# Kernel optimization log

Hardware: AMD Instinct MI355X
Metric: run time of the kernel (lower is better)

The kernel has to match this reference:

```python
import jax, jax.numpy as jnp
import numpy as np
import math

D_IN, D_MODEL, N_HEADS, DIM_HEAD, NB_FEAT, N_CLASSES = 24, 512, 8, 64, 266, 10
FF_DIM = 4 * D_MODEL  # performer-pytorch FeedForward mult=4
LN_EPS = 1e-5
B, N = 16, 2048


def gaussian_orthogonal(key, nb_rows, nb_cols):
    # FAVOR+ gaussian orthogonal random matrix (scaling=0: chi-distributed row norms)
    n_blocks = nb_rows // nb_cols + 1
    keys = jax.random.split(key, n_blocks + 1)
    blocks = []
    for i in range(n_blocks):
        q, _ = jnp.linalg.qr(jax.random.normal(keys[i], (nb_cols, nb_cols)))
        blocks.append(q.T)
    mat = jnp.concatenate(blocks, axis=0)[:nb_rows]
    multiplier = jnp.linalg.norm(jax.random.normal(keys[-1], (nb_rows, nb_cols)), axis=1)
    return multiplier[:, None] * mat


def layer_norm(x, g, b):
    mu = jnp.mean(x, axis=-1, keepdims=True)
    var = jnp.var(x, axis=-1, keepdims=True)
    return (x - mu) * jax.lax.rsqrt(var + LN_EPS) * g + b


def softmax_kernel(data, proj, is_query, eps=1e-4):
    # FAVOR+ positive random features approximating the softmax kernel
    data_norm = data.shape[-1] ** -0.25
    ratio = proj.shape[0] ** -0.5
    dd = jnp.einsum('bhnd,fd->bhnf', data * data_norm, proj)  # [B,H,N,F]
    diag = 0.5 * jnp.sum(data * data, axis=-1, keepdims=True) * (data_norm ** 2)
    if is_query:
        m = jax.lax.stop_gradient(jnp.max(dd, axis=-1, keepdims=True))
    else:
        m = jax.lax.stop_gradient(jnp.max(dd))
    return ratio * (jnp.exp(dd - diag - m) + eps)


def setup_inputs() -> dict:
    key = jax.random.key(0)
    ks = jax.random.split(key, 24)

    def linw(k, fi, fo):
        bnd = 1.0 / math.sqrt(fi)
        return jax.random.uniform(k, (fi, fo), minval=-bnd, maxval=bnd, dtype=jnp.float32)

    def linb(k, fi, fo):
        bnd = 1.0 / math.sqrt(fi)
        return jax.random.uniform(k, (fo,), minval=-bnd, maxval=bnd, dtype=jnp.float32)

    return {
        'x': jax.random.normal(ks[0], (B, N, D_IN), dtype=jnp.float32),
        'enc_w': linw(ks[1], D_IN, D_MODEL), 'enc_b': linb(ks[2], D_IN, D_MODEL),
        'ln1_g': jnp.ones((D_MODEL,), jnp.float32), 'ln1_b': jnp.zeros((D_MODEL,), jnp.float32),
        'wq': linw(ks[3], D_MODEL, D_MODEL), 'bq': linb(ks[4], D_MODEL, D_MODEL),
        'wk': linw(ks[5], D_MODEL, D_MODEL), 'bk': linb(ks[6], D_MODEL, D_MODEL),
        'wv': linw(ks[7], D_MODEL, D_MODEL), 'bv': linb(ks[8], D_MODEL, D_MODEL),
        'wo': linw(ks[9], D_MODEL, D_MODEL), 'bo': linb(ks[10], D_MODEL, D_MODEL),
        'proj': gaussian_orthogonal(ks[11], NB_FEAT, DIM_HEAD).astype(jnp.float32),
        'ln2_g': jnp.ones((D_MODEL,), jnp.float32), 'ln2_b': jnp.zeros((D_MODEL,), jnp.float32),
        'ff_w1': linw(ks[12], D_MODEL, FF_DIM), 'ff_b1': linb(ks[13], D_MODEL, FF_DIM),
        'ff_w2': linw(ks[14], FF_DIM, D_MODEL), 'ff_b2': linb(ks[15], FF_DIM, D_MODEL),
        'mlp_w1': linw(ks[16], D_MODEL, D_MODEL), 'mlp_b1': linb(ks[17], D_MODEL, D_MODEL),
        'mlp_w2': linw(ks[18], D_MODEL, N_CLASSES), 'mlp_b2': linb(ks[19], D_MODEL, N_CLASSES),
    }


def reference(x, enc_w, enc_b, ln1_g, ln1_b, wq, bq, wk, bk, wv, bv, wo, bo, proj,
              ln2_g, ln2_b, ff_w1, ff_b1, ff_w2, ff_b2, mlp_w1, mlp_b1, mlp_w2, mlp_b2):
    b, n, _ = x.shape
    h = (x @ enc_w + enc_b) * math.sqrt(D_MODEL)  # [B,N,D]

    # --- Performer layer: PreLN + FAVOR+ self-attention ---
    y = layer_norm(h, ln1_g, ln1_b)
    split = lambda t: t.reshape(b, n, N_HEADS, DIM_HEAD).transpose(0, 2, 1, 3)  # [B,H,N,Dh]
    q = split(y @ wq + bq)
    k = split(y @ wk + bk)
    v = split(y @ wv + bv)
    qp = softmax_kernel(q, proj, is_query=True)   # [B,H,N,F]
    kp = softmax_kernel(k, proj, is_query=False)  # [B,H,N,F]
    # non-causal linear attention
    k_sum = kp.sum(axis=2)                                   # [B,H,F]
    d_inv = 1.0 / jnp.einsum('bhnf,bhf->bhn', qp, k_sum)     # [B,H,N]
    ctx = jnp.einsum('bhnf,bhnd->bhfd', kp, v)               # [B,H,F,Dh]
    attn = jnp.einsum('bhnf,bhfd,bhn->bhnd', qp, ctx, d_inv)
    attn = attn.transpose(0, 2, 1, 3).reshape(b, n, D_MODEL)
    h = h + attn @ wo + bo

    y = layer_norm(h, ln2_g, ln2_b)
    h = h + jax.nn.gelu(y @ ff_w1 + ff_b1, approximate=False) @ ff_w2 + ff_b2

    # --- max pool over sequence + MLP head ---
    p = jnp.max(h, axis=1)  # [B,D]
    return jax.nn.relu(p @ mlp_w1 + mlp_b1) @ mlp_w2 + mlp_b2  # [B,n_classes]
```

## Files before the change

kernel.cpp:

```cpp
#include <hip/hip_runtime.h>
#include <math.h>

typedef unsigned short u16;
typedef __bf16 bf16x8 __attribute__((ext_vector_type(8)));
typedef float f32x4 __attribute__((ext_vector_type(4)));
typedef u16 u16x8 __attribute__((ext_vector_type(8)));

#define DEVI static __device__ __forceinline__

#define NB 16
#define SEQ 2048
#define DM 512
#define DH 64
#define NF 266
#define NFP 288
#define NFQ 296
#define FFD 2048
#define ROWS (NB*SEQ)
#define SQRT_DM 22.62741699796952f
#define DATA_NORM 0.3535533905932738f
#define RATIO 0.0613139073f
#define KEPS 1e-4f

DEVI u16 f2b(float f){
  union{float f; unsigned u;} c; c.f=f;
  unsigned r = c.u + 0x7FFFu + ((c.u>>16)&1u);
  return (u16)(r>>16);
}
DEVI float b2f(u16 v){
  union{unsigned u; float f;} c; c.u = ((unsigned)v)<<16; return c.f;
}

DEVI f32x4 MFMA(bf16x8 a, bf16x8 b, f32x4 c){
  return __builtin_amdgcn_mfma_f32_16x16x32_bf16(a,b,c,0,0,0);
}

DEVI void async16(void* lds, const void* g){
  __builtin_amdgcn_global_load_lds(
      (const __attribute__((address_space(1))) unsigned*)g,
      (__attribute__((address_space(3))) unsigned*)lds, 16, 0, 0);
}

DEVI void atomicMaxF(float* a, float v){
  if (v >= 0.f) atomicMax((int*)a, __float_as_int(v));
  else          atomicMin((unsigned*)a, (unsigned)__float_as_int(v));
}

DEVI bf16x8 ldb8(const u16* p){ return *(const bf16x8*)p; }

DEVI float erf_fast(float u){
  float au = fabsf(u);
  float tt = __builtin_amdgcn_rcpf(1.f + 0.3275911f*au);
  float poly = tt*(0.254829592f + tt*(-0.284496736f + tt*(1.421413741f + tt*(-1.453152027f + tt*1.061405429f))));
  float er = 1.f - poly*__expf(-u*u);
  return copysignf(er, u);
}

template<int EPI>
__launch_bounds__(256,2)
__global__ void gemm_tn(const u16* __restrict__ A, int lda,
                        const u16* __restrict__ Bt, int ldb,
                        const float* __restrict__ bias,
                        float* __restrict__ resid,
                        u16* __restrict__ Cb,
                        int N, int K)
{
  __shared__ u16 As[2][128*32];
  __shared__ u16 Bs[2][128*32];
  const int t = threadIdx.x;
  const int ntn = N >> 7;
  int bid = blockIdx.x;
  const int nwg = gridDim.x;
  if ((nwg & 7) == 0){ int qq = nwg >> 3; bid = (bid & 7)*qq + (bid >> 3); }
  const int bm = bid / ntn, bn = bid % ntn;
  const int w = t>>6, l = t&63, lr = l&15, lg = l>>4;
  const int wr = (w>>1)*64, wc = (w&1)*64;
  const u16* ga = A  + (size_t)(bm*128 + (t>>2))*lda + (t&3)*8;
  const u16* gb = Bt + (size_t)(bn*128 + (t>>2))*ldb + (t&3)*8;
  const int nk = K >> 5;
  f32x4 acc[4][4];
  #pragma unroll
  for (int i=0;i<4;i++)
    #pragma unroll
    for (int j=0;j<4;j++) acc[i][j]=(f32x4){0.f,0.f,0.f,0.f};

  async16(&As[0][t*8], ga);
  async16(&As[0][64*32 + t*8], ga + (size_t)64*lda);
  async16(&Bs[0][t*8], gb);
  async16(&Bs[0][64*32 + t*8], gb + (size_t)64*ldb);

  for (int kt=0; kt<nk; ++kt){
    __syncthreads();
    if (kt+1 < nk){
      const u16* ga2 = ga + (kt+1)*32;
      const u16* gb2 = gb + (kt+1)*32;
      int nbuf = (kt+1)&1;
      async16(&As[nbuf][t*8], ga2);
      async16(&As[nbuf][64*32 + t*8], ga2 + (size_t)64*lda);
      async16(&Bs[nbuf][t*8], gb2);
      async16(&Bs[nbuf][64*32 + t*8], gb2 + (size_t)64*ldb);
    }
    const u16* as = As[kt&1];
    const u16* bs = Bs[kt&1];
    bf16x8 af[4], bff[4];
    #pragma unroll
    for (int i=0;i<4;i++) af[i]  = ldb8(&as[(wr + i*16 + lr)*32 + lg*8]);
    #pragma unroll
    for (int i=0;i<4;i++) bff[i] = ldb8(&bs[(wc + i*16 + lr)*32 + lg*8]);
    #pragma unroll
    for (int i=0;i<4;i++)
      #pragma unroll
      for (int j=0;j<4;j++)
        acc[i][j] = MFMA(af[i], bff[j], acc[i][j]);
  }

  const int r0 = bm*128 + wr + lg*4;
  const int c0 = bn*128 + wc + lr;
  #pragma unroll
  for (int i=0;i<4;i++){
    #pragma unroll
    for (int j=0;j<4;j++){
      #pragma unroll
      for (int q=0;q<4;q++){
        int r = r0 + i*16 + q;
        int c = c0 + j*16;
        float v = acc[i][j][q] + bias[c];
        if (EPI==2) v = 0.5f*v*(1.f + erf_fast(v*0.70710678f));
        size_t idx = (size_t)r*N + c;
        if (EPI==3) resid[idx] = resid[idx] + v;
        else        Cb[idx] = f2b(v);
      }
    }
  }
}

__launch_bounds__(256)
__global__ void k_prep(const float* __restrict__ wq, const float* __restrict__ wk,
                       const float* __restrict__ wv, const float* __restrict__ wo,
                       const float* __restrict__ ffw1, const float* __restrict__ ffw2,
                       const float* __restrict__ proj, const float* __restrict__ bk,
                       const float* __restrict__ bv,
                       u16* __restrict__ wqT, u16* __restrict__ wkvT, u16* __restrict__ woT,
                       u16* __restrict__ f1T, u16* __restrict__ f2T, u16* __restrict__ pjn,
                       float* __restrict__ kvb, float* __restrict__ pbuf)
{
  int bid = blockIdx.x, t = threadIdx.x;
  if (bid < 3072){
    const float* src; u16* dst; int R, C, tile;
    if      (bid < 256){ src=wq;  dst=wqT;          R=512; C=512;  tile=bid; }
    else if (bid < 512){ src=wk;  dst=wkvT;         R=512; C=512;  tile=bid-256; }
    else if (bid < 768){ src=wv;  dst=wkvT+262144;  R=512; C=512;  tile=bid-512; }
    else if (bid <1024){ src=wo;  dst=woT;          R=512; C=512;  tile=bid-768; }
    else if (bid <2048){ src=ffw1;dst=f1T;          R=512; C=2048; tile=bid-1024; }
    else               { src=ffw2;dst=f2T;          R=2048;C=512;  tile=bid-2048; }
    int ntc = C>>5;
    int tr = tile/ntc, tc = tile%ntc;
    __shared__ float tl[32][33];
    int r = t>>5, c = t&31;
    #pragma unroll
    for (int it=0; it<4; ++it)
      tl[r+it*8][c] = src[(size_t)(tr*32 + r + it*8)*C + tc*32 + c];
    __syncthreads();
    #pragma unroll
    for (int it=0; it<4; ++it)
      dst[(size_t)(tc*32 + r + it*8)*R + tr*32 + c] = f2b(tl[c][r+it*8]);
    return;
  }
  int i = (bid-3072)*256 + t;
  if (i < NFP*DH){ int f=i>>6, d=i&63; pjn[i] = f2b(f<NF ? proj[(size_t)f*64+d]*DATA_NORM : 0.f); return; }
  i -= NFP*DH;
  if (i < 1024){ kvb[i] = (i<512)? bk[i] : bv[i-512]; return; }
  i -= 1024;
  if (i < NB*DM){ pbuf[i] = -INFINITY; return; }
}

__global__ void k_signal(float* out, float v){
  if (threadIdx.x==0 && blockIdx.x==0) out[0] = v;
}

__launch_bounds__(256)
__global__ void k_encode_ln(const float* __restrict__ x, const float* __restrict__ ew,
                            const float* __restrict__ eb, const float* __restrict__ lgw,
                            const float* __restrict__ lbw, float* __restrict__ h,
                            u16* __restrict__ y)
{
  int w = threadIdx.x>>6, l = threadIdx.x&63;
  int row = blockIdx.x*4 + w;
  const float* xr = x + (size_t)row*24;
  float xv[24];
  #pragma unroll
  for (int k=0;k<24;k++) xv[k] = xr[k];
  int c0 = l*8;
  float a[8] = {0,0,0,0,0,0,0,0};
  #pragma unroll
  for (int k=0;k<24;k++){
    const float* wp = ew + (size_t)k*DM + c0;
    #pragma unroll
    for (int c=0;c<8;c++) a[c] += xv[k]*wp[c];
  }
  float s=0.f, s2=0.f;
  #pragma unroll
  for (int c=0;c<8;c++){
    a[c] = (a[c] + eb[c0+c]) * SQRT_DM;
    s += a[c]; s2 += a[c]*a[c];
  }
  #pragma unroll
  for (int m=1;m<64;m<<=1){ s += __shfl_xor(s,m); s2 += __shfl_xor(s2,m); }
  float mu = s*(1.f/DM);
  float rs = rsqrtf(s2*(1.f/DM) - mu*mu + 1e-5f);
  float* hr = h + (size_t)row*DM + c0;
  u16 yv[8];
  #pragma unroll
  for (int c=0;c<8;c++){
    hr[c] = a[c];
    yv[c] = f2b((a[c]-mu)*rs*lgw[c0+c] + lbw[c0+c]);
  }
  *(uint4*)(y + (size_t)row*DM + c0) = *(const uint4*)yv;
}

__launch_bounds__(256)
__global__ void k_ln(const float* __restrict__ h, const float* __restrict__ lgw,
                     const float* __restrict__ lbw, u16* __restrict__ y)
{
  int w = threadIdx.x>>6, l = threadIdx.x&63;
  int row = blockIdx.x*4 + w;
  int c0 = l*8;
  const float* hr = h + (size_t)row*DM + c0;
  float a[8];
  *(float4*)&a[0] = *(const float4*)hr;
  *(float4*)&a[4] = *(const float4*)(hr+4);
  float s=0.f, s2=0.f;
  #pragma unroll
  for (int c=0;c<8;c++){ s += a[c]; s2 += a[c]*a[c]; }
  #pragma unroll
  for (int m=1;m<64;m<<=1){ s += __shfl_xor(s,m); s2 += __shfl_xor(s2,m); }
  float mu = s*(1.f/DM);
  float rs = rsqrtf(s2*(1.f/DM) - mu*mu + 1e-5f);
  u16 yv[8];
  #pragma unroll
  for (int c=0;c<8;c++) yv[c] = f2b((a[c]-mu)*rs*lgw[c0+c] + lbw[c0+c]);
  *(uint4*)(y + (size_t)row*DM + c0) = *(const uint4*)yv;
}

__launch_bounds__(256,1)
__global__ void k_kmax(const u16* __restrict__ kv, const u16* __restrict__ pjn,
                       float* __restrict__ mkpart)
{
  __shared__ float red[4];
  int t = threadIdx.x, w = t>>6, l = t&63, lr = l&15, lg = l>>4;
  int bh = blockIdx.x>>3, tile = blockIdx.x&7;
  int b = bh>>3, hd = bh&7;
  int row0 = tile*256 + w*64;
  bf16x8 pf0[17], pf1[17];
  #pragma unroll
  for (int f=0; f<17; ++f){
    const u16* pb = pjn + (f*16 + lr)*64 + lg*8;
    pf0[f] = ldb8(pb); pf1[f] = ldb8(pb+32);
  }
  bf16x8 a0[4], a1[4];
  #pragma unroll
  for (int it=0; it<4; ++it){
    const u16* kb = kv + ((size_t)(b*SEQ + row0 + it*16 + lr)*1024 + hd*64 + lg*8);
    a0[it] = ldb8(kb); a1[it] = ldb8(kb+32);
  }
  float vmax = -3e38f;
  #pragma unroll
  for (int it=0; it<4; ++it){
    #pragma unroll
    for (int f=0; f<17; ++f){
      f32x4 z = (f32x4){0.f,0.f,0.f,0.f};
      z = MFMA(a0[it], pf0[f], z);
      z = MFMA(a1[it], pf1[f], z);
      if (f*16 + lr < NF){
        #pragma unroll
        for (int j=0;j<4;j++) vmax = fmaxf(vmax, z[j]);
      }
    }
  }
  #pragma unroll
  for (int m=1;m<64;m<<=1) vmax = fmaxf(vmax, __shfl_xor(vmax,m));
  if (l==0) red[w] = vmax;
  __syncthreads();
  if (t==0) mkpart[blockIdx.x] = fmaxf(fmaxf(red[0],red[1]), fmaxf(red[2],red[3]));
}

__global__ void k_kmax_red(const float* __restrict__ mkpart, float* __restrict__ mk){
  __shared__ float red[4];
  int t = threadIdx.x, w = t>>6, l = t&63;
  float v = fmaxf(fmaxf(mkpart[t], mkpart[t+256]), fmaxf(mkpart[t+512], mkpart[t+768]));
  #pragma unroll
  for (int m=1;m<64;m<<=1) v = fmaxf(v, __shfl_xor(v,m));
  if (l==0) red[w] = v;
  __syncthreads();
  if (t==0) mk[0] = fmaxf(fmaxf(red[0],red[1]), fmaxf(red[2],red[3]));
}

__launch_bounds__(256,2)
__global__ void k_kpctx(const u16* __restrict__ kv, const u16* __restrict__ pjn,
                        const float* __restrict__ mkp,
                        u16* __restrict__ ctxp, float* __restrict__ ksump)
{
  __shared__ u16 pjs[272*64];
  __shared__ u16 vT[DH*32];
  __shared__ u16 kpT[NFP*32];
  __shared__ float dbuf[4][16];
  int t = threadIdx.x, w = t>>6, l = t&63, lr = l&15, lg = l>>4;
  int bh = blockIdx.x>>2, seg = blockIdx.x&3;
  int b = bh>>3, hd = bh&7;
  int mw = w>>1, fh = (w&1)*9;
  float mk = *mkp;

  for (int i=t; i<2176; i+=256){
    int row = i>>3, cin = i&7;
    *(uint4*)&pjs[row*64 + ((cin ^ (row&7))<<3)] = ((const uint4*)pjn)[i];
  }

  f32x4 ctxa[18];
  #pragma unroll
  for (int f=0;f<18;f++) ctxa[f]=(f32x4){0.f,0.f,0.f,0.f};
  float ksa[9];
  #pragma unroll
  for (int i=0;i<9;i++) ksa[i]=0.f;

  for (int ch=0; ch<16; ++ch){
    int n0 = seg*512 + ch*32;
    __syncthreads();
    {
      int nl = t>>3, d0 = (t&7)*8;
      const u16* vsrc = kv + ((size_t)(b*SEQ + n0 + nl)*1024 + 512 + hd*64 + d0);
      uint4 vv = *(const uint4*)vsrc;
      const u16* vp = (const u16*)&vv;
      #pragma unroll
      for (int i=0;i<8;i++){
        int row = d0+i;
        vT[row*32 + (((nl>>3) ^ ((row>>1)&3))<<3) + (nl&7)] = vp[i];
      }
    }
    const u16* kb = kv + ((size_t)(b*SEQ + n0 + mw*16 + lr)*1024 + hd*64 + lg*8);
    bf16x8 a0 = ldb8(kb), a1 = ldb8(kb+32);
    float sq = 0.f;
    #pragma unroll
    for (int i=0;i<8;i++){ float u0=(float)a0[i], u1=(float)a1[i]; sq += u0*u0 + u1*u1; }
    sq += __shfl_xor(sq,16); sq += __shfl_xor(sq,32);
    if (l<16) dbuf[w][l] = sq*0.0625f;
    #pragma unroll
    for (int ff=0; ff<9; ++ff){
      int f = fh + ff;
      f32x4 z = (f32x4){0.f,0.f,0.f,0.f};
      if (f < 17){
        int row = f*16 + lr;
        const u16* pb0 = pjs + row*64 + ((lg ^ (lr&7))<<3);
        const u16* pb1 = pjs + row*64 + (((lg+4) ^ (lr&7))<<3);
        z = MFMA(a0, ldb8(pb0), z);
        z = MFMA(a1, ldb8(pb1), z);
      }
      float kp0 = RATIO*(__expf(z[0] - dbuf[w][lg*4+0] - mk) + KEPS);
      float kp1 = RATIO*(__expf(z[1] - dbuf[w][lg*4+1] - mk) + KEPS);
      float kp2 = RATIO*(__expf(z[2] - dbuf[w][lg*4+2] - mk) + KEPS);
      float kp3 = RATIO*(__expf(z[3] - dbuf[w][lg*4+3] - mk) + KEPS);
      ksa[ff] += kp0 + kp1 + kp2 + kp3;
      ushort4 kw;
      kw.x = f2b(kp0); kw.y = f2b(kp1); kw.z = f2b(kp2); kw.w = f2b(kp3);
      int row = f*16 + lr;
      int wch = (mw*2 + (lg>>1)) ^ ((row>>1)&3);
      *(ushort4*)&kpT[row*32 + (wch<<3) + ((lg&1)<<2)] = kw;
    }
    __syncthreads();
    int rr = w*16 + lr;
    bf16x8 av = ldb8(&vT[rr*32 + ((lg ^ ((rr>>1)&3))<<3)]);
    #pragma unroll
    for (int f=0;f<18;f++){
      int row = f*16 + lr;
      ctxa[f] = MFMA(av, ldb8(&kpT[row*32 + ((lg ^ ((row>>1)&3))<<3)]), ctxa[f]);
    }
  }

  __syncthreads();
  {
    float* tb = (w&1) ? (float*)pjs : (float*)kpT;
    u16* dstq = ctxp + (((size_t)seg*128 + bh)*DH + w*16)*NFP;
    #pragma unroll
    for (int r=0; r<2; ++r){
      if ((w>>1) == r){
        #pragma unroll
        for (int f=0;f<18;f++)
          #pragma unroll
          for (int j=0;j<4;j++)
            tb[(lg*4+j)*NFP + f*16 + lr] = ctxa[f][j];
        asm volatile("s_waitcnt lgkmcnt(0)" ::: "memory");
        #pragma unroll
        for (int k=0;k<9;k++){
          int c = k*64 + l;
          f32x4 v0 = *(const f32x4*)(tb + c*8);
          f32x4 v1 = *(const f32x4*)(tb + c*8 + 4);
          u16x8 o;
          o[0]=f2b(v0[0]); o[1]=f2b(v0[1]); o[2]=f2b(v0[2]); o[3]=f2b(v0[3]);
          o[4]=f2b(v1[0]); o[5]=f2b(v1[1]); o[6]=f2b(v1[2]); o[7]=f2b(v1[3]);
          *(u16x8*)(dstq + c*8) = o;
        }
      }
      __syncthreads();
    }
  }
  #pragma unroll
  for (int ff=0;ff<9;ff++){
    float v = ksa[ff];
    v += __shfl_xor(v,16); v += __shfl_xor(v,32);
    if (l<16) ksump[((size_t)seg*128 + bh)*NFP + (fh+ff)*16 + l] = v;
  }
}

__global__ void k_reduce(const u16* __restrict__ ctxp, const float* __restrict__ ksump,
                         u16* __restrict__ ctxb, float* __restrict__ ksum)
{
  const size_t CT = (size_t)128*DH*NFP;
  const size_t KT = (size_t)128*NFP;
  size_t i = (size_t)blockIdx.x*256 + threadIdx.x;
  if (i < CT){
    float s = b2f(ctxp[i]) + b2f(ctxp[i+CT]) + b2f(ctxp[i+2*CT]) + b2f(ctxp[i+3*CT]);
    ctxb[i] = f2b(s);
  } else if (i < CT + KT){
    size_t j = i - CT;
    ksum[j] = ksump[j] + ksump[j+KT] + ksump[j+2*KT] + ksump[j+3*KT];
  }
}

__launch_bounds__(256,2)
__global__ void k_qp_attn(const u16* __restrict__ q, const u16* __restrict__ pjn,
                          const u16* __restrict__ ctxb, const float* __restrict__ ksum,
                          u16* __restrict__ attn)
{
  __shared__ u16 qp[64*NFQ];
  __shared__ float dnb[64];
  __shared__ float dgb[64];
  int t = threadIdx.x, w = t>>6, l = t&63, lr = l&15, lg = l>>4;
  int bh = blockIdx.x>>5, tile = blockIdx.x&31;
  int b = bh>>3, hd = bh&7;
  int n0 = tile*64;
  const u16* qb = q + ((size_t)(b*SEQ + n0 + w*16 + lr)*DM + hd*64 + lg*8);
  bf16x8 a0 = ldb8(qb), a1 = ldb8(qb+32);
  float sq = 0.f;
  #pragma unroll
  for (int i=0;i<8;i++){ float u0=(float)a0[i], u1=(float)a1[i]; sq += u0*u0 + u1*u1; }
  sq += __shfl_xor(sq,16); sq += __shfl_xor(sq,32);
  if (l<16) dgb[w*16+l] = sq*0.0625f;

  f32x4 dd[18];
  #pragma unroll
  for (int f=0;f<18;f++){
    const u16* pb = pjn + (f*16 + lr)*64 + lg*8;
    f32x4 z = (f32x4){0.f,0.f,0.f,0.f};
    z = MFMA(a0, ldb8(pb), z);
    dd[f] = MFMA(a1, ldb8(pb+32), z);
  }
  float mj[4] = {-3e38f,-3e38f,-3e38f,-3e38f};
  #pragma unroll
  for (int f=0;f<18;f++){
    if (f*16 + lr < NF){
      #pragma unroll
      for (int j=0;j<4;j++) mj[j] = fmaxf(mj[j], dd[f][j]);
    }
  }
  #pragma unroll
  for (int m=1;m<16;m<<=1)
    #pragma unroll
    for (int j=0;j<4;j++) mj[j] = fmaxf(mj[j], __shfl_xor(mj[j],m));
  float dg[4];
  #pragma unroll
  for (int j=0;j<4;j++) dg[j] = dgb[w*16 + lg*4 + j];
  float den[4] = {0.f,0.f,0.f,0.f};
  #pragma unroll
  for (int f=0;f<18;f++){
    int col = f*16 + lr;
    float ks = ksum[(size_t)bh*NFP + col];
    #pragma unroll
    for (int j=0;j<4;j++){
      float qv = 0.f;
      if (col < NF) qv = RATIO*(__expf(dd[f][j] - dg[j] - mj[j]) + KEPS);
      den[j] += qv*ks;
      qp[(w*16 + lg*4 + j)*NFQ + col] = f2b(qv);
    }
  }
  #pragma unroll
  for (int m=1;m<16;m<<=1)
    #pragma unroll
    for (int j=0;j<4;j++) den[j] += __shfl_xor(den[j],m);
  if (lr==0){
    #pragma unroll
    for (int j=0;j<4;j++) dnb[w*16 + lg*4 + j] = den[j];
  }
  __syncthreads();
  bf16x8 aq[9];
  #pragma unroll
  for (int k9=0;k9<9;k9++) aq[k9] = ldb8(&qp[(w*16 + lr)*NFQ + k9*32 + lg*8]);
  f32x4 oacc[4];
  #pragma unroll
  for (int d=0;d<4;d++) oacc[d]=(f32x4){0.f,0.f,0.f,0.f};
  const u16* cbase = ctxb + (size_t)bh*DH*NFP;
  #pragma unroll
  for (int d=0;d<4;d++)
    #pragma unroll
    for (int k9=0;k9<9;k9++)
      oacc[d] = MFMA(aq[k9], ldb8(&cbase[(d*16 + lr)*NFP + k9*32 + lg*8]), oacc[d]);
  float di[4];
  #pragma unroll
  for (int j=0;j<4;j++) di[j] = 1.f/dnb[w*16 + lg*4 + j];
  #pragma unroll
  for (int d=0;d<4;d++)
    #pragma unroll
    for (int j=0;j<4;j++){
      int n = n0 + w*16 + lg*4 + j;
      attn[((size_t)(b*SEQ + n))*DM + hd*64 + d*16 + lr] = f2b(oacc[d][j]*di[j]);
    }
}

__global__ void k_maxpool(const float* __restrict__ h, float* __restrict__ p){
  int bi = blockIdx.x;
  int b = bi>>5, half = (bi>>4)&1, seg = bi&15;
  int c = half*256 + threadIdx.x;
  const float* hp = h + ((size_t)b*SEQ + seg*128)*DM + c;
  float m = -3e38f;
  for (int n=0;n<128;n++) m = fmaxf(m, hp[(size_t)n*DM]);
  atomicMaxF(&p[b*DM + c], m);
}

__launch_bounds__(256)
__global__ void k_head(const float* __restrict__ p, const float* __restrict__ w1,
                       const float* __restrict__ b1, const float* __restrict__ w2,
                       const float* __restrict__ b2, float* __restrict__ out)
{
  __shared__ float z[DM];
  __shared__ float pr[DM];
  int b = blockIdx.x, t = threadIdx.x;
  pr[t] = p[(size_t)b*DM + t];
  pr[t+256] = p[(size_t)b*DM + t + 256];
  __syncthreads();
  for (int c=t; c<DM; c+=256){
    float a = b1[c];
    for (int k=0;k<DM;k++) a += pr[k]*w1[(size_t)k*DM + c];
    z[c] = fmaxf(a, 0.f);
  }
  __syncthreads();
  if (t < 10){
    float a = b2[t];
    for (int k=0;k<DM;k++) a += z[k]*w2[(size_t)k*10 + t];
    out[b*10 + t] = a;
  }
}

static inline size_t align256(size_t x){ return (x+255)&~(size_t)255; }

extern "C" void kernel_launch(void* const* d_in, const int* in_sizes, int n_in,
                              void* d_out, int out_size, void* d_ws, size_t ws_size,
                              hipStream_t stream)
{
  (void)in_sizes; (void)n_in; (void)out_size;
  const float* x     = (const float*)d_in[0];
  const float* enc_w = (const float*)d_in[1];
  const float* enc_b = (const float*)d_in[2];
  const float* ln1_g = (const float*)d_in[3];
  const float* ln1_b = (const float*)d_in[4];
  const float* wq    = (const float*)d_in[5];
  const float* bq    = (const float*)d_in[6];
  const float* wk    = (const float*)d_in[7];
  const float* bk    = (const float*)d_in[8];
  const float* wv    = (const float*)d_in[9];
  const float* bv    = (const float*)d_in[10];
  const float* wo    = (const float*)d_in[11];
  const float* bo    = (const float*)d_in[12];
  const float* proj  = (const float*)d_in[13];
  const float* ln2_g = (const float*)d_in[14];
  const float* ln2_b = (const float*)d_in[15];
  const float* ff_w1 = (const float*)d_in[16];
  const float* ff_b1 = (const float*)d_in[17];
  const float* ff_w2 = (const float*)d_in[18];
  const float* ff_b2 = (const float*)d_in[19];
  const float* mw1   = (const float*)d_in[20];
  const float* mb1   = (const float*)d_in[21];
  const float* mw2   = (const float*)d_in[22];
  const float* mb2   = (const float*)d_in[23];

  char* base = (char*)d_ws;
  size_t off = 0;
  auto alloc = [&](size_t bytes)->void*{ void* r = base + off; off = align256(off + bytes); return r; };
  float* h     = (float*)alloc((size_t)ROWS*DM*4);
  u16*   slotA = (u16*)  alloc((size_t)ROWS*DM*2);
  u16*   slotB = (u16*)  alloc((size_t)ROWS*1024*2);
  u16*   wqT   = (u16*)  alloc((size_t)512*512*2);
  u16*   wkvT  = (u16*)  alloc((size_t)1024*512*2);
  u16*   woT   = (u16*)  alloc((size_t)512*512*2);
  u16*   f1T   = (u16*)  alloc((size_t)2048*512*2);
  u16*   f2T   = (u16*)  alloc((size_t)512*2048*2);
  u16*   pjn   = (u16*)  alloc((size_t)NFP*DH*2);
  float* kvb   = (float*)alloc(1024*4);
  float* mk    = (float*)alloc(256);
  float* mkpart= (float*)alloc(1024*4);
  u16*   ctxp  = (u16*)  alloc((size_t)4*128*DH*NFP*2);
  float* ksump = (float*)alloc((size_t)4*128*NFP*4);
  u16*   ctxb  = (u16*)  alloc((size_t)128*DH*NFP*2);
  float* ksum  = (float*)alloc((size_t)128*NFP*4);
  float* pbuf  = (float*)alloc((size_t)NB*DM*4);

  if (off > ws_size){
    k_signal<<<1,64,0,stream>>>((float*)d_out, (float)ws_size);
    return;
  }

  u16* y    = slotA;
  u16* attn = slotA;
  u16* kvB  = slotB;
  u16* qB   = slotB;
  u16* ffb  = slotB;

  k_prep<<<3180,256,0,stream>>>(wq, wk, wv, wo, ff_w1, ff_w2, proj, bk, bv,
                                wqT, wkvT, woT, f1T, f2T, pjn, kvb, pbuf);

  k_encode_ln<<<ROWS/4,256,0,stream>>>(x, enc_w, enc_b, ln1_g, ln1_b, h, y);
  gemm_tn<1><<<(ROWS/128)*(1024/128),256,0,stream>>>(y,512, wkvT,512, kvb, nullptr, kvB, 1024, 512);
  k_kmax<<<1024,256,0,stream>>>(kvB, pjn, mkpart);
  k_kmax_red<<<1,256,0,stream>>>(mkpart, mk);
  k_kpctx<<<512,256,0,stream>>>(kvB, pjn, mk, ctxp, ksump);
  k_reduce<<<9360,256,0,stream>>>(ctxp, ksump, ctxb, ksum);
  gemm_tn<1><<<(ROWS/128)*(512/128),256,0,stream>>>(y,512, wqT,512, bq, nullptr, qB, 512, 512);
  k_qp_attn<<<128*32,256,0,stream>>>(qB, pjn, ctxb, ksum, attn);
  gemm_tn<3><<<(ROWS/128)*(512/128),256,0,stream>>>(attn,512, woT,512, bo, h, nullptr, 512, 512);
  k_ln<<<ROWS/4,256,0,stream>>>(h, ln2_g, ln2_b, y);
  for (int c2=0;c2<2;c2++){
    const u16* ych = y + (size_t)c2*16384*512;
    float*     hch = h + (size_t)c2*16384*512;
    gemm_tn<2><<<(16384/128)*(2048/128),256,0,stream>>>(ych,512, f1T,512, ff_b1, nullptr, ffb, 2048, 512);
    gemm_tn<3><<<(16384/128)*(512/128),256,0,stream>>>(ffb,2048, f2T,2048, ff_b2, hch, nullptr, 512, 2048);
  }
  k_maxpool<<<NB*32,256,0,stream>>>(h, pbuf);
  k_head<<<NB,256,0,stream>>>(pbuf, mw1, mb1, mw2, mb2, (float*)d_out);
}
```

Before: 689.0 us.

## Keep qp features in registers via transposed MFMA and lane shuffles in qp_attn

Rewrites the query-feature/attention kernel to swap MFMA operand order so each lane holds one query row. The qp tile then stays in registers as packed bf16 and is redistributed with cross-lane shuffles instead of going through LDS and a block barrier. It recomputes the projection matmul in a second pass rather than keeping 18 accumulators live, and raises launch bounds to 4 blocks per SM. Output stores become vectorized ushort4. The cost is extra MFMA work and many shuffles, traded for less LDS traffic, no __syncthreads, and higher occupancy.

```diff
diff --git a/kernel.cpp b/kernel.cpp
--- a/kernel.cpp
+++ b/kernel.cpp
@@ -14,7 +14,6 @@
 #define DH 64
 #define NF 266
 #define NFP 288
-#define NFQ 296
 #define FFD 2048
 #define ROWS (NB*SEQ)
 #define SQRT_DM 22.62741699796952f
@@ -29,6 +28,11 @@
 }
 DEVI float b2f(u16 v){
   union{unsigned u; float f;} c; c.u = ((unsigned)v)<<16; return c.f;
+}
+DEVI unsigned cvtpk(float a, float b){
+  unsigned r;
+  asm("v_cvt_pk_bf16_f32 %0, %1, %2" : "=v"(r) : "v"(a), "v"(b));
+  return r;
 }
 
 DEVI f32x4 MFMA(bf16x8 a, bf16x8 b, f32x4 c){
@@ -425,14 +429,11 @@
   }
 }
 
-__launch_bounds__(256,2)
+__launch_bounds__(256,4)
 __global__ void k_qp_attn(const u16* __restrict__ q, const u16* __restrict__ pjn,
                           const u16* __restrict__ ctxb, const float* __restrict__ ksum,
                           u16* __restrict__ attn)
 {
-  __shared__ u16 qp[64*NFQ];
-  __shared__ float dnb[64];
-  __shared__ float dgb[64];
   int t = threadIdx.x, w = t>>6, l = t&63, lr = l&15, lg = l>>4;
   int bh = blockIdx.x>>5, tile = blockIdx.x&31;
   int b = bh>>3, hd = bh&7;
@@ -443,75 +444,83 @@
   #pragma unroll
   for (int i=0;i<8;i++){ float u0=(float)a0[i], u1=(float)a1[i]; sq += u0*u0 + u1*u1; }
   sq += __shfl_xor(sq,16); sq += __shfl_xor(sq,32);
-  if (l<16) dgb[w*16+l] = sq*0.0625f;
-
-  f32x4 dd[18];
-  #pragma unroll
-  for (int f=0;f<18;f++){
-    const u16* pb = pjn + (f*16 + lr)*64 + lg*8;
+  float dg = sq*0.0625f;
+
+  float mj = -3e38f;
+  #pragma unroll
+  for (int ft=0; ft<17; ++ft){
+    const u16* pb = pjn + (ft*16 + lr)*64 + lg*8;
     f32x4 z = (f32x4){0.f,0.f,0.f,0.f};
-    z = MFMA(a0, ldb8(pb), z);
-    dd[f] = MFMA(a1, ldb8(pb+32), z);
-  }
-  float mj[4] = {-3e38f,-3e38f,-3e38f,-3e38f};
-  #pragma unroll
-  for (int f=0;f<18;f++){
-    if (f*16 + lr < NF){
+    z = MFMA(ldb8(pb), a0, z);
+    z = MFMA(ldb8(pb+32), a1, z);
+    if (ft < 16){
       #pragma unroll
-      for (int j=0;j<4;j++) mj[j] = fmaxf(mj[j], dd[f][j]);
-    }
-  }
-  #pragma unroll
-  for (int m=1;m<16;m<<=1)
-    #pragma unroll
-    for (int j=0;j<4;j++) mj[j] = fmaxf(mj[j], __shfl_xor(mj[j],m));
-  float dg[4];
-  #pragma unroll
-  for (int j=0;j<4;j++) dg[j] = dgb[w*16 + lg*4 + j];
-  float den[4] = {0.f,0.f,0.f,0.f};
-  #pragma unroll
-  for (int f=0;f<18;f++){
-    int col = f*16 + lr;
-    float ks = ksum[(size_t)bh*NFP + col];
+      for (int j=0;j<4;j++) mj = fmaxf(mj, z[j]);
+    } else {
+      #pragma unroll
+      for (int j=0;j<4;j++) if (lg*4+j < 10) mj = fmaxf(mj, z[j]);
+    }
+  }
+  mj = fmaxf(mj, __shfl_xor(mj,16));
+  mj = fmaxf(mj, __shfl_xor(mj,32));
+
+  unsigned p0[18], p1[18];
+  float den = 0.f;
+  const float* ksb = ksum + (size_t)bh*NFP;
+  #pragma unroll
+  for (int ft=0; ft<18; ++ft){
+    f32x4 z = (f32x4){0.f,0.f,0.f,0.f};
+    if (ft < 17){
+      const u16* pb = pjn + (ft*16 + lr)*64 + lg*8;
+      z = MFMA(ldb8(pb), a0, z);
+      z = MFMA(ldb8(pb+32), a1, z);
+    }
+    f32x4 ks4 = *(const f32x4*)(ksb + ft*16 + lg*4);
+    int fb = ft*16 + lg*4;
+    float qv[4];
     #pragma unroll
     for (int j=0;j<4;j++){
-      float qv = 0.f;
-      if (col < NF) qv = RATIO*(__expf(dd[f][j] - dg[j] - mj[j]) + KEPS);
-      den[j] += qv*ks;
-      qp[(w*16 + lg*4 + j)*NFQ + col] = f2b(qv);
-    }
-  }
-  #pragma unroll
-  for (int m=1;m<16;m<<=1)
-    #pragma unroll
-    for (int j=0;j<4;j++) den[j] += __shfl_xor(den[j],m);
-  if (lr==0){
-    #pragma unroll
-    for (int j=0;j<4;j++) dnb[w*16 + lg*4 + j] = den[j];
-  }
-  __syncthreads();
-  bf16x8 aq[9];
-  #pragma unroll
-  for (int k9=0;k9<9;k9++) aq[k9] = ldb8(&qp[(w*16 + lr)*NFQ + k9*32 + lg*8]);
+      qv[j] = (fb + j < NF) ? RATIO*(__expf(z[j] - dg - mj) + KEPS) : 0.f;
+      den += qv[j]*ks4[j];
+    }
+    p0[ft] = cvtpk(qv[0], qv[1]);
+    p1[ft] = cvtpk(qv[2], qv[3]);
+  }
+  den += __shfl_xor(den,16); den += __shfl_xor(den,32);
+  float di = 1.f/den;
+
+  int s0 = ((lg&1)<<5) + lr;
+  int s1 = s0 + 16;
+  bool hi = (l >= 32);
   f32x4 oacc[4];
   #pragma unroll
   for (int d=0;d<4;d++) oacc[d]=(f32x4){0.f,0.f,0.f,0.f};
   const u16* cbase = ctxb + (size_t)bh*DH*NFP;
   #pragma unroll
-  for (int d=0;d<4;d++)
-    #pragma unroll
-    for (int k9=0;k9<9;k9++)
-      oacc[d] = MFMA(aq[k9], ldb8(&cbase[(d*16 + lr)*NFP + k9*32 + lg*8]), oacc[d]);
-  float di[4];
-  #pragma unroll
-  for (int j=0;j<4;j++) di[j] = 1.f/dnb[w*16 + lg*4 + j];
-  #pragma unroll
-  for (int d=0;d<4;d++)
-    #pragma unroll
-    for (int j=0;j<4;j++){
-      int n = n0 + w*16 + lg*4 + j;
-      attn[((size_t)(b*SEQ + n))*DM + hd*64 + d*16 + lr] = f2b(oacc[d][j]*di[j]);
-    }
+  for (int k9=0;k9<9;k9++){
+    int te = 2*k9, to = te+1;
+    unsigned e0 = (unsigned)__shfl((int)p0[te], s0), o0 = (unsigned)__shfl((int)p0[to], s0);
+    unsigned e1 = (unsigned)__shfl((int)p1[te], s0), o1 = (unsigned)__shfl((int)p1[to], s0);
+    unsigned e2 = (unsigned)__shfl((int)p0[te], s1), o2 = (unsigned)__shfl((int)p0[to], s1);
+    unsigned e3 = (unsigned)__shfl((int)p1[te], s1), o3 = (unsigned)__shfl((int)p1[to], s1);
+    union { unsigned u[4]; bf16x8 v; } bw;
+    bw.u[0] = hi ? o0 : e0;
+    bw.u[1] = hi ? o1 : e1;
+    bw.u[2] = hi ? o2 : e2;
+    bw.u[3] = hi ? o3 : e3;
+    #pragma unroll
+    for (int d=0;d<4;d++)
+      oacc[d] = MFMA(ldb8(&cbase[(d*16 + lr)*NFP + k9*32 + lg*8]), bw.v, oacc[d]);
+  }
+
+  u16* ab = attn + ((size_t)(b*SEQ + n0 + w*16 + lr))*DM + hd*64 + lg*4;
+  #pragma unroll
+  for (int d=0;d<4;d++){
+    ushort4 o;
+    o.x = f2b(oacc[d][0]*di); o.y = f2b(oacc[d][1]*di);
+    o.z = f2b(oacc[d][2]*di); o.w = f2b(oacc[d][3]*di);
+    *(ushort4*)(ab + d*16) = o;
+  }
 }
 
 __global__ void k_maxpool(const float* __restrict__ h, float* __restrict__ p){
```

Measured after the change: 810.5 us. 1.18x slower.
